# Kernel optimization log

Hardware: AMD Instinct MI355X
Metric: run time of the kernel (lower is better)

The kernel has to match this reference:

```python
import jax, jax.numpy as jnp
import numpy as np

NUM_HEADS = 16
HEAD_DIM = 64
DIM = NUM_HEADS * HEAD_DIM
ROPE_BASE = 10000.0
EPS = 1e-6


def rotate_half(x):
    # pairs (x0,x1) -> (-x1, x0), interleaved on last dim
    x_even = x[..., ::2]
    x_odd = x[..., 1::2]
    return jnp.stack((-x_odd, x_even), axis=-1).reshape(x.shape)


def apply_rope(q, k, positions, base=ROPE_BASE):
    d = q.shape[-1]
    inv_freq = 1.0 / (base ** (jnp.arange(0, d, 2, dtype=jnp.float32) / d))
    angles = positions.astype(jnp.float32)[..., None] * inv_freq  # [B, L, d/2]
    cos = jnp.repeat(jnp.cos(angles), 2, axis=-1).astype(q.dtype)[:, None, :, :]  # [B,1,L,d]
    sin = jnp.repeat(jnp.sin(angles), 2, axis=-1).astype(q.dtype)[:, None, :, :]
    return q * cos + rotate_half(q) * sin, k * cos + rotate_half(k) * sin


def per_head_layernorm(x, weight):
    # x: [B, H, L, d]; weight: [H, d]; bias is zeros (qkv_bias=False)
    mu = jnp.mean(x, axis=-1, keepdims=True)
    var = jnp.mean(jnp.square(x - mu), axis=-1, keepdims=True)
    xn = (x - mu) * jax.lax.rsqrt(var + EPS)
    return xn * weight[None, :, None, :]


def setup_inputs() -> dict:
    key = jax.random.key(0)
    k1, k2, k3, k4, k5 = jax.random.split(key, 5)
    B, L = 2, 2048
    x = jax.random.normal(k1, (B, L, DIM), dtype=jnp.float32)
    mask = jnp.ones((B, L, L), dtype=bool)
    positions = jnp.broadcast_to(jnp.arange(L, dtype=jnp.int64 if jax.config.jax_enable_x64 else jnp.int32), (B, L))
    s = 1.0 / np.sqrt(DIM)
    W_qkv = jax.random.normal(k2, (DIM, 3 * DIM), dtype=jnp.float32) * s
    W_out = jax.random.normal(k3, (DIM, DIM), dtype=jnp.float32) * s
    qn_w = jnp.ones((NUM_HEADS, HEAD_DIM), dtype=jnp.float32)
    kn_w = jnp.ones((NUM_HEADS, HEAD_DIM), dtype=jnp.float32)
    return {"x": x, "mask": mask, "positions": positions,
            "W_qkv": W_qkv, "W_out": W_out, "qn_w": qn_w, "kn_w": kn_w}


def reference(x, mask, positions, W_qkv, W_out, qn_w, kn_w):
    B, L, D = x.shape
    scale = HEAD_DIM ** -0.5
    qkv = x @ W_qkv  # [B, L, 3D]
    qkv = qkv.reshape(B, L, 3, NUM_HEADS, HEAD_DIM)
    qkv = jnp.transpose(qkv, (2, 0, 3, 1, 4))  # [3, B, H, L, d]
    q, k, v = qkv[0], qkv[1], qkv[2]
    q = per_head_layernorm(q, qn_w)
    k = per_head_layernorm(k, kn_w)
    q, k = apply_rope(q, k, positions)
    attn = jnp.einsum('bhqd,bhkd->bhqk', q, k) * scale  # [B, H, L, L]
    attn = jnp.where(mask[:, None, :, :], attn, -jnp.inf)
    attn = jax.nn.softmax(attn, axis=-1)
    out = jnp.einsum('bhqk,bhkd->bhqd', attn, v)  # [B, H, L, d]
    out = jnp.transpose(out, (0, 2, 1, 3)).reshape(B, L, D)
    return out @ W_out
```

## Files before the change

### kernel.cpp

```cpp
#include <hip/hip_runtime.h>


typedef __bf16 bf16x8 __attribute__((ext_vector_type(8)));
typedef __bf16 bf16x2 __attribute__((ext_vector_type(2)));
typedef float f32x4 __attribute__((ext_vector_type(4)));

#define QSCALE 0.1803368802f

__device__ __forceinline__ float bf2f(unsigned short u) {
  unsigned int v = ((unsigned int)u) << 16;
  float f;
  __builtin_memcpy(&f, &v, 4);
  return f;
}
__device__ __forceinline__ unsigned short f2bf(float f) {
  unsigned int v;
  __builtin_memcpy(&v, &f, 4);
  v += 0x7fffu + ((v >> 16) & 1u);
  return (unsigned short)(v >> 16);
}
__device__ __forceinline__ unsigned short f2bf_hw(float f) {
  __bf16 h = (__bf16)f;
  unsigned short u;
  __builtin_memcpy(&u, &h, 2);
  return u;
}
__device__ __forceinline__ unsigned int pack2(float a, float b) {
  bf16x2 t;
  t[0] = (__bf16)a;
  t[1] = (__bf16)b;
  unsigned int u;
  __builtin_memcpy(&u, &t, 4);
  return u;
}
__device__ __forceinline__ void gl_lds16(const unsigned short* g, unsigned short* l) {
  __builtin_amdgcn_global_load_lds(
      (const __attribute__((address_space(1))) unsigned int*)g,
      (__attribute__((address_space(3))) unsigned int*)l, 16, 0, 0);
}

__global__ __launch_bounds__(256) void prep(
    const float* __restrict__ x, const float* __restrict__ W_qkv,
    const float* __restrict__ W_out, const int* __restrict__ positions,
    unsigned short* __restrict__ xb,
    unsigned short* __restrict__ Wt_qkv, unsigned short* __restrict__ Wt_out,
    float2* __restrict__ lut) {
  __shared__ float tile[64][65];
  const int bid = blockIdx.x, t = threadIdx.x;
  if (bid < 4096) {
    int i = (bid * 256 + t) * 4;
    float4 v = *reinterpret_cast<const float4*>(x + i);
    ushort4 o;
    o.x = f2bf(v.x); o.y = f2bf(v.y); o.z = f2bf(v.z); o.w = f2bf(v.w);
    *reinterpret_cast<ushort4*>(xb + i) = o;
    return;
  }
  if (bid >= 5120) {
    int idx = (bid - 5120) * 256 + t;
    int m = idx >> 5, p = idx & 31;
    float pos = (float)positions[m];
    float invf = __builtin_amdgcn_exp2f(-(float)(2 * p) * (13.2877124f / 64.0f));
    float rev = pos * invf * 0.15915494f;
    rev -= floorf(rev);
    lut[idx] = make_float2(__builtin_amdgcn_cosf(rev), __builtin_amdgcn_sinf(rev));
    return;
  }
  const float* W; unsigned short* Wt; int Nd, bn, bk;
  if (bid < 4864) {
    int id = bid - 4096; W = W_qkv; Wt = Wt_qkv; Nd = 3072; bn = id % 48; bk = id / 48;
  } else {
    int id = bid - 4864; W = W_out; Wt = Wt_out; Nd = 1024; bn = id % 16; bk = id / 16;
  }
  const int Kd = 1024;
#pragma unroll
  for (int i = 0; i < 16; i++) {
    int idx = i * 256 + t;
    int k = idx >> 6, n = idx & 63;
    tile[k][n] = W[(size_t)(bk * 64 + k) * Nd + bn * 64 + n];
  }
  __syncthreads();
#pragma unroll
  for (int i = 0; i < 16; i++) {
    int idx = i * 256 + t;
    int n = idx >> 6, k = idx & 63;
    Wt[(size_t)(bn * 64 + n) * Kd + bk * 64 + k] = f2bf(tile[k][n]);
  }
}

__global__ __launch_bounds__(256) void gemm_qkv(
    const unsigned short* __restrict__ A,
    const unsigned short* __restrict__ Bt,
    const float* __restrict__ qn_w, const float* __restrict__ kn_w,
    const float2* __restrict__ lut,
    unsigned short* __restrict__ Qr,
    unsigned short* __restrict__ Kr,
    unsigned short* __restrict__ Vt, int K) {
  __shared__ __align__(16) unsigned short As[128 * 32];
  __shared__ __align__(16) unsigned short Bs[128 * 32];
  const int tid = threadIdx.x;
  const int lane = tid & 63, wid = tid >> 6;
  const int quad = lane >> 4, l16 = lane & 15;
  const int wr = wid >> 1, wc = wid & 1;
  const int bn = blockIdx.x, bm = blockIdx.y;
  const unsigned short* Ab = A + (size_t)bm * 128 * K;
  const unsigned short* Bb = Bt + (size_t)bn * 128 * K;

  f32x4 acc[4][4] = {};

  const int c0 = tid, c1 = tid + 256;
  const int ar0 = c0 >> 2, ag0 = ((c0 & 3) ^ ((ar0 >> 1) & 3)) * 8;
  const int ar1 = c1 >> 2, ag1 = ((c1 & 3) ^ ((ar1 >> 1) & 3)) * 8;

  for (int k0 = 0; k0 < K; k0 += 32) {
    gl_lds16(Ab + (size_t)ar0 * K + k0 + ag0, &As[c0 * 8]);
    gl_lds16(Ab + (size_t)ar1 * K + k0 + ag1, &As[c1 * 8]);
    gl_lds16(Bb + (size_t)ar0 * K + k0 + ag0, &Bs[c0 * 8]);
    gl_lds16(Bb + (size_t)ar1 * K + k0 + ag1, &Bs[c1 * 8]);
    __syncthreads();
    bf16x8 af[4], bfr[4];
#pragma unroll
    for (int i = 0; i < 4; i++) {
      int m = wr * 64 + i * 16 + l16;
      af[i] = *reinterpret_cast<const bf16x8*>(&As[m * 32 + ((quad ^ ((m >> 1) & 3)) * 8)]);
    }
#pragma unroll
    for (int j = 0; j < 4; j++) {
      int n = wc * 64 + j * 16 + l16;
      bfr[j] = *reinterpret_cast<const bf16x8*>(&Bs[n * 32 + ((quad ^ ((n >> 1) & 3)) * 8)]);
    }
#pragma unroll
    for (int i = 0; i < 4; i++)
#pragma unroll
      for (int j = 0; j < 4; j++)
        acc[i][j] = __builtin_amdgcn_mfma_f32_16x16x32_bf16(af[i], bfr[j], acc[i][j], 0, 0, 0);
    __syncthreads();
  }

  const int sec = bn >> 3;
  const int h = (bn & 7) * 2 + wc;
  const int b = bm >> 4;
  if (sec < 2) {
    const float* gw = sec ? kn_w : qn_w;
    unsigned short* dst = sec ? Kr : Qr;
    const float oscale = sec ? 1.0f : QSCALE;
    float w4[4];
#pragma unroll
    for (int j = 0; j < 4; j++) w4[j] = gw[h * 64 + j * 16 + l16];
#pragma unroll
    for (int i = 0; i < 4; i++)
#pragma unroll
      for (int r = 0; r < 4; r++) {
        int m = bm * 128 + wr * 64 + i * 16 + quad * 4 + r;
        int l = m & 2047;
        const float2* lrow = lut + m * 32;
        float2 cs4[4];
#pragma unroll
        for (int j = 0; j < 4; j++) cs4[j] = lrow[j * 8 + (l16 >> 1)];
        float sum = acc[i][0][r] + acc[i][1][r] + acc[i][2][r] + acc[i][3][r];
        float sq = acc[i][0][r] * acc[i][0][r] + acc[i][1][r] * acc[i][1][r] +
                   acc[i][2][r] * acc[i][2][r] + acc[i][3][r] * acc[i][3][r];
#pragma unroll
        for (int off = 1; off < 16; off <<= 1) {
          sum += __shfl_xor(sum, off);
          sq += __shfl_xor(sq, off);
        }
        float mu = sum * (1.0f / 64.0f);
        float var = sq * (1.0f / 64.0f) - mu * mu;
        float rs = rsqrtf(fmaxf(var, 0.0f) + 1e-6f);
#pragma unroll
        for (int j = 0; j < 4; j++) {
          float y = (acc[i][j][r] - mu) * rs * w4[j];
          float p = __shfl_xor(y, 1);
          float o = (l16 & 1) ? (y * cs4[j].x + p * cs4[j].y)
                              : (y * cs4[j].x - p * cs4[j].y);
          dst[((size_t)(b * 16 + h) * 2048 + l) * 64 + j * 16 + l16] = f2bf(o * oscale);
        }
      }
  } else {
#pragma unroll
    for (int i = 0; i < 4; i++) {
      int lp = (bm * 128 + wr * 64 + (i >> 1) * 32 + quad * 8 + (i & 1) * 4) & 2047;
#pragma unroll
      for (int j = 0; j < 4; j++) {
        int d = j * 16 + l16;
        uint2 v;
        v.x = pack2(acc[i][j][0], acc[i][j][1]);
        v.y = pack2(acc[i][j][2], acc[i][j][3]);
        *reinterpret_cast<uint2*>(&Vt[((size_t)(b * 16 + h) * 64 + d) * 2048 + lp]) = v;
      }
    }
  }
}

__global__ __launch_bounds__(512, 4) void attn_kernel(
    const unsigned short* __restrict__ Q,
    const unsigned short* __restrict__ K,
    const unsigned short* __restrict__ Vt,
    unsigned short* __restrict__ O) {
  __shared__ __align__(16) unsigned short Ks[2][2][64 * 64];
  __shared__ __align__(16) unsigned short Vs[2][2][64 * 64];

  int id = blockIdx.x;
  const int qt = id & 15; id >>= 4;
  const int h = id & 15;  const int b = id >> 4;
  const int tid = threadIdx.x;
  const int lane = tid & 63, wid = tid >> 6;
  const int half = wid >> 2, wg = wid & 3;
  const int quad = lane >> 4, l16 = lane & 15;

  const unsigned short* Qb = Q + (size_t)(b * 16 + h) * 2048 * 64;
  const unsigned short* Kb = K + (size_t)(b * 16 + h) * 2048 * 64;
  const unsigned short* Vb = Vt + (size_t)(b * 16 + h) * 64 * 2048;

  const int qbase = qt * 128 + wg * 32;
  bf16x8 qf[2][2];
#pragma unroll
  for (int g = 0; g < 2; g++)
#pragma unroll
    for (int d = 0; d < 2; d++)
      qf[g][d] = *reinterpret_cast<const bf16x8*>(
          &Qb[(size_t)(qbase + g * 16 + l16) * 64 + d * 32 + quad * 8]);

  f32x4 o[2][4] = {};
  float lsum[2] = {0.f, 0.f};

  const int ltid = tid & 255;
  const int c0 = ltid, c1 = ltid + 256;
  const int r0 = c0 >> 3, g0 = ((c0 & 7) ^ (r0 & 7)) * 8;
  const int r1 = c1 >> 3, g1 = ((c1 & 7) ^ (r1 & 7)) * 8;
  const int kb0 = half * 1024;

  gl_lds16(&Kb[(size_t)(kb0 + r0) * 64 + g0], &Ks[half][0][c0 * 8]);
  gl_lds16(&Kb[(size_t)(kb0 + r1) * 64 + g1], &Ks[half][0][c1 * 8]);
  gl_lds16(&Vb[(size_t)r0 * 2048 + kb0 + g0], &Vs[half][0][c0 * 8]);
  gl_lds16(&Vb[(size_t)r1 * 2048 + kb0 + g1], &Vs[half][0][c1 * 8]);

  for (int kt = 0; kt < 16; kt++) {
    const int cur = kt & 1;
    __syncthreads();
    if (kt + 1 < 16) {
      const int ko = kb0 + (kt + 1) * 64, nb = cur ^ 1;
      gl_lds16(&Kb[(size_t)(ko + r0) * 64 + g0], &Ks[half][nb][c0 * 8]);
      gl_lds16(&Kb[(size_t)(ko + r1) * 64 + g1], &Ks[half][nb][c1 * 8]);
      gl_lds16(&Vb[(size_t)r0 * 2048 + ko + g0], &Vs[half][nb][c0 * 8]);
      gl_lds16(&Vb[(size_t)r1 * 2048 + ko + g1], &Vs[half][nb][c1 * 8]);
    }
    const unsigned short* Kc = Ks[half][cur];
    const unsigned short* Vc = Vs[half][cur];

    bf16x8 kf[4][2];
#pragma unroll
    for (int kg = 0; kg < 4; kg++)
#pragma unroll
      for (int d = 0; d < 2; d++) {
        int row = kg * 16 + l16;
        kf[kg][d] = *reinterpret_cast<const bf16x8*>(
            &Kc[row * 64 + (((d * 4 + quad) ^ (row & 7)) * 8)]);
      }
    bf16x8 vf[4][2];
#pragma unroll
    for (int i = 0; i < 4; i++)
#pragma unroll
      for (int c = 0; c < 2; c++) {
        int row = i * 16 + l16;
        vf[i][c] = *reinterpret_cast<const bf16x8*>(
            &Vc[row * 64 + (((c * 4 + quad) ^ (row & 7)) * 8)]);
      }

#pragma unroll
    for (int g = 0; g < 2; g++) {
      f32x4 s4[4] = {};
#pragma unroll
      for (int kg = 0; kg < 4; kg++) {
        s4[kg] = __builtin_amdgcn_mfma_f32_16x16x32_bf16(kf[kg][0], qf[g][0], s4[kg], 0, 0, 0);
        s4[kg] = __builtin_amdgcn_mfma_f32_16x16x32_bf16(kf[kg][1], qf[g][1], s4[kg], 0, 0, 0);
      }
      float pv[4][4];
#pragma unroll
      for (int kg = 0; kg < 4; kg++)
#pragma unroll
        for (int r = 0; r < 4; r++) {
          float e = __builtin_amdgcn_exp2f(s4[kg][r]);
          pv[kg][r] = e;
          lsum[g] += e;
        }
#pragma unroll
      for (int c = 0; c < 2; c++) {
        union { unsigned int u[4]; bf16x8 v; } pa;
        pa.u[0] = pack2(pv[c * 2][0], pv[c * 2][1]);
        pa.u[1] = pack2(pv[c * 2][2], pv[c * 2][3]);
        pa.u[2] = pack2(pv[c * 2 + 1][0], pv[c * 2 + 1][1]);
        pa.u[3] = pack2(pv[c * 2 + 1][2], pv[c * 2 + 1][3]);
#pragma unroll
        for (int i = 0; i < 4; i++)
          o[g][i] = __builtin_amdgcn_mfma_f32_16x16x32_bf16(pa.v, vf[i][c], o[g][i], 0, 0, 0);
      }
    }
  }

#pragma unroll
  for (int g = 0; g < 2; g++) {
    lsum[g] += __shfl_xor(lsum[g], 16);
    lsum[g] += __shfl_xor(lsum[g], 32);
  }

  __syncthreads();
  float* Om = (float*)&Ks[0][0][0];
  float* Lm = (float*)&Vs[0][0][0];
  if (half == 0) {
#pragma unroll
    for (int g = 0; g < 2; g++) {
#pragma unroll
      for (int i = 0; i < 4; i++)
#pragma unroll
        for (int r = 0; r < 4; r++)
          Om[(wg * 32 + g * 16 + quad * 4 + r) * 64 + i * 16 + l16] = o[g][i][r];
      if (quad == 0) Lm[wg * 32 + g * 16 + l16] = lsum[g];
    }
  }
  __syncthreads();
  if (half == 1) {
#pragma unroll
    for (int g = 0; g < 2; g++) {
      float lt = lsum[g] + Lm[wg * 32 + g * 16 + l16];
#pragma unroll
      for (int r = 0; r < 4; r++) {
        float inv = 1.0f / __shfl(lt, quad * 4 + r);
        int q = qbase + g * 16 + quad * 4 + r;
#pragma unroll
        for (int i = 0; i < 4; i++) {
          float sum = o[g][i][r] + Om[(wg * 32 + g * 16 + quad * 4 + r) * 64 + i * 16 + l16];
          O[((size_t)(b * 2048 + q)) * 1024 + h * 64 + i * 16 + l16] = f2bf_hw(sum * inv);
        }
      }
    }
  }
}

__global__ __launch_bounds__(256) void gemm_out(
    const unsigned short* __restrict__ A,
    const unsigned short* __restrict__ Bt,
    float* __restrict__ C, int M, int N, int K) {
  __shared__ __align__(16) unsigned short As[2][128 * 32];
  __shared__ __align__(16) unsigned short Bs[2][64 * 32];
  const int tid = threadIdx.x;
  const int lane = tid & 63, wid = tid >> 6;
  const int quad = lane >> 4, l16 = lane & 15;
  const int bn = blockIdx.x, bm = blockIdx.y;
  const unsigned short* Ab = A + (size_t)bm * 128 * K;
  const unsigned short* Bb = Bt + (size_t)bn * 64 * K;

  f32x4 acc[2][4] = {};

  const int c0 = tid, c1 = tid + 256;
  const int ar0 = c0 >> 2, ag0 = ((c0 & 3) ^ ((ar0 >> 1) & 3)) * 8;
  const int ar1 = c1 >> 2, ag1 = ((c1 & 3) ^ ((ar1 >> 1) & 3)) * 8;
  const int br = tid >> 2, bg = ((tid & 3) ^ ((br >> 1) & 3)) * 8;

  gl_lds16(Ab + (size_t)ar0 * K + ag0, &As[0][c0 * 8]);
  gl_lds16(Ab + (size_t)ar1 * K + ag1, &As[0][c1 * 8]);
  gl_lds16(Bb + (size_t)br * K + bg, &Bs[0][tid * 8]);

  const int iters = K >> 5;
  for (int it = 0; it < iters; it++) {
    const int cur = it & 1;
    __syncthreads();
    if (it + 1 < iters) {
      const int k0 = (it + 1) << 5, nb = cur ^ 1;
      gl_lds16(Ab + (size_t)ar0 * K + k0 + ag0, &As[nb][c0 * 8]);
      gl_lds16(Ab + (size_t)ar1 * K + k0 + ag1, &As[nb][c1 * 8]);
      gl_lds16(Bb + (size_t)br * K + k0 + bg, &Bs[nb][tid * 8]);
    }
    const unsigned short* Ac = As[cur];
    const unsigned short* Bc = Bs[cur];
    bf16x8 af[2], bfr[4];
#pragma unroll
    for (int i = 0; i < 2; i++) {
      int m = wid * 32 + i * 16 + l16;
      af[i] = *reinterpret_cast<const bf16x8*>(&Ac[m * 32 + ((quad ^ ((m >> 1) & 3)) * 8)]);
    }
#pragma unroll
    for (int j = 0; j < 4; j++) {
      int n = j * 16 + l16;
      bfr[j] = *reinterpret_cast<const bf16x8*>(&Bc[n * 32 + ((quad ^ ((n >> 1) & 3)) * 8)]);
    }
#pragma unroll
    for (int i = 0; i < 2; i++)
#pragma unroll
      for (int j = 0; j < 4; j++)
        acc[i][j] = __builtin_amdgcn_mfma_f32_16x16x32_bf16(af[i], bfr[j], acc[i][j], 0, 0, 0);
  }
#pragma unroll
  for (int i = 0; i < 2; i++)
#pragma unroll
    for (int j = 0; j < 4; j++)
#pragma unroll
      for (int r = 0; r < 4; r++) {
        int m = bm * 128 + wid * 32 + i * 16 + quad * 4 + r;
        int n = bn * 64 + j * 16 + l16;
        C[(size_t)m * N + n] = acc[i][j][r];
      }
}

extern "C" void kernel_launch(void* const* d_in, const int* in_sizes, int n_in,
                              void* d_out, int out_size, void* d_ws, size_t ws_size,
                              hipStream_t stream) {
  (void)in_sizes; (void)n_in; (void)out_size; (void)ws_size;
  const float* x     = (const float*)d_in[0];
  const int*   pos   = (const int*)d_in[2];
  const float* W_qkv = (const float*)d_in[3];
  const float* W_out = (const float*)d_in[4];
  const float* qn_w  = (const float*)d_in[5];
  const float* kn_w  = (const float*)d_in[6];
  float*       out   = (float*)d_out;

  char* ws = (char*)d_ws;
  unsigned short* xb     = (unsigned short*)(ws);
  unsigned short* Qr     = (unsigned short*)(ws + 8388608);
  unsigned short* Kr     = (unsigned short*)(ws + 16777216);
  unsigned short* Vt     = (unsigned short*)(ws + 25165824);
  unsigned short* Wt_qkv = (unsigned short*)(ws + 33554432);
  unsigned short* Wt_out = (unsigned short*)(ws + 39845888);
  float2*         lut    = (float2*)(ws + 41943040);
  unsigned short* attn_o = xb;

  prep<<<5632, 256, 0, stream>>>(x, W_qkv, W_out, pos, xb, Wt_qkv, Wt_out, lut);
  gemm_qkv<<<dim3(24, 32), 256, 0, stream>>>(xb, Wt_qkv, qn_w, kn_w, lut, Qr, Kr, Vt, 1024);
  attn_kernel<<<512, 512, 0, stream>>>(Qr, Kr, Vt, attn_o);
  gemm_out<<<dim3(16, 32), 256, 0, stream>>>(attn_o, Wt_out, out, 4096, 1024, 1024);
}
```

Measured before the change: 212.2 us.

## Double-buffer QKV GEMM LDS tiles and compute softmax row sums via MFMA

The QKV projection GEMM now uses double-buffered LDS tiles: the next K-slice is prefetched while MFMAs consume the current one, which also removes one barrier per iteration. In the attention kernel, the per-lane scalar accumulation of exp values plus the final cross-lane shuffles is replaced by an extra MFMA against a vector of ones. That MFMA yields row sums directly in the accumulator layout. The changes double the GEMM's LDS footprint, which may lower occupancy, and the row sums are now built from bf16-rounded probabilities rather than fp32 values.

```diff
diff --git a/kernel.cpp b/kernel.cpp
--- a/kernel.cpp
+++ b/kernel.cpp
@@ -95,8 +95,8 @@
     unsigned short* __restrict__ Qr,
     unsigned short* __restrict__ Kr,
     unsigned short* __restrict__ Vt, int K) {
-  __shared__ __align__(16) unsigned short As[128 * 32];
-  __shared__ __align__(16) unsigned short Bs[128 * 32];
+  __shared__ __align__(16) unsigned short As[2][128 * 32];
+  __shared__ __align__(16) unsigned short Bs[2][128 * 32];
   const int tid = threadIdx.x;
   const int lane = tid & 63, wid = tid >> 6;
   const int quad = lane >> 4, l16 = lane & 15;
@@ -111,29 +111,40 @@
   const int ar0 = c0 >> 2, ag0 = ((c0 & 3) ^ ((ar0 >> 1) & 3)) * 8;
   const int ar1 = c1 >> 2, ag1 = ((c1 & 3) ^ ((ar1 >> 1) & 3)) * 8;
 
-  for (int k0 = 0; k0 < K; k0 += 32) {
-    gl_lds16(Ab + (size_t)ar0 * K + k0 + ag0, &As[c0 * 8]);
-    gl_lds16(Ab + (size_t)ar1 * K + k0 + ag1, &As[c1 * 8]);
-    gl_lds16(Bb + (size_t)ar0 * K + k0 + ag0, &Bs[c0 * 8]);
-    gl_lds16(Bb + (size_t)ar1 * K + k0 + ag1, &Bs[c1 * 8]);
+  gl_lds16(Ab + (size_t)ar0 * K + ag0, &As[0][c0 * 8]);
+  gl_lds16(Ab + (size_t)ar1 * K + ag1, &As[0][c1 * 8]);
+  gl_lds16(Bb + (size_t)ar0 * K + ag0, &Bs[0][c0 * 8]);
+  gl_lds16(Bb + (size_t)ar1 * K + ag1, &Bs[0][c1 * 8]);
+
+  const int iters = K >> 5;
+  for (int it = 0; it < iters; it++) {
+    const int cur = it & 1;
     __syncthreads();
+    if (it + 1 < iters) {
+      const int k0 = (it + 1) << 5, nb = cur ^ 1;
+      gl_lds16(Ab + (size_t)ar0 * K + k0 + ag0, &As[nb][c0 * 8]);
+      gl_lds16(Ab + (size_t)ar1 * K + k0 + ag1, &As[nb][c1 * 8]);
+      gl_lds16(Bb + (size_t)ar0 * K + k0 + ag0, &Bs[nb][c0 * 8]);
+      gl_lds16(Bb + (size_t)ar1 * K + k0 + ag1, &Bs[nb][c1 * 8]);
+    }
+    const unsigned short* Ac = As[cur];
+    const unsigned short* Bc = Bs[cur];
     bf16x8 af[4], bfr[4];
 #pragma unroll
     for (int i = 0; i < 4; i++) {
       int m = wr * 64 + i * 16 + l16;
-      af[i] = *reinterpret_cast<const bf16x8*>(&As[m * 32 + ((quad ^ ((m >> 1) & 3)) * 8)]);
+      af[i] = *reinterpret_cast<const bf16x8*>(&Ac[m * 32 + ((quad ^ ((m >> 1) & 3)) * 8)]);
     }
 #pragma unroll
     for (int j = 0; j < 4; j++) {
       int n = wc * 64 + j * 16 + l16;
-      bfr[j] = *reinterpret_cast<const bf16x8*>(&Bs[n * 32 + ((quad ^ ((n >> 1) & 3)) * 8)]);
+      bfr[j] = *reinterpret_cast<const bf16x8*>(&Bc[n * 32 + ((quad ^ ((n >> 1) & 3)) * 8)]);
     }
 #pragma unroll
     for (int i = 0; i < 4; i++)
 #pragma unroll
       for (int j = 0; j < 4; j++)
         acc[i][j] = __builtin_amdgcn_mfma_f32_16x16x32_bf16(af[i], bfr[j], acc[i][j], 0, 0, 0);
-    __syncthreads();
   }
 
   const int sec = bn >> 3;
@@ -221,8 +232,12 @@
       qf[g][d] = *reinterpret_cast<const bf16x8*>(
           &Qb[(size_t)(qbase + g * 16 + l16) * 64 + d * 32 + quad * 8]);
 
+  bf16x8 ones8;
+#pragma unroll
+  for (int i = 0; i < 8; i++) ones8[i] = (__bf16)1.0f;
+
   f32x4 o[2][4] = {};
-  float lsum[2] = {0.f, 0.f};
+  f32x4 lacc[2] = {};
 
   const int ltid = tid & 255;
   const int c0 = ltid, c1 = ltid + 256;
@@ -279,11 +294,8 @@
 #pragma unroll
       for (int kg = 0; kg < 4; kg++)
 #pragma unroll
-        for (int r = 0; r < 4; r++) {
-          float e = __builtin_amdgcn_exp2f(s4[kg][r]);
-          pv[kg][r] = e;
-          lsum[g] += e;
-        }
+        for (int r = 0; r < 4; r++)
+          pv[kg][r] = __builtin_amdgcn_exp2f(s4[kg][r]);
 #pragma unroll
       for (int c = 0; c < 2; c++) {
         union { unsigned int u[4]; bf16x8 v; } pa;
@@ -291,17 +303,12 @@
         pa.u[1] = pack2(pv[c * 2][2], pv[c * 2][3]);
         pa.u[2] = pack2(pv[c * 2 + 1][0], pv[c * 2 + 1][1]);
         pa.u[3] = pack2(pv[c * 2 + 1][2], pv[c * 2 + 1][3]);
+        lacc[g] = __builtin_amdgcn_mfma_f32_16x16x32_bf16(pa.v, ones8, lacc[g], 0, 0, 0);
 #pragma unroll
         for (int i = 0; i < 4; i++)
           o[g][i] = __builtin_amdgcn_mfma_f32_16x16x32_bf16(pa.v, vf[i][c], o[g][i], 0, 0, 0);
       }
     }
-  }
-
-#pragma unroll
-  for (int g = 0; g < 2; g++) {
-    lsum[g] += __shfl_xor(lsum[g], 16);
-    lsum[g] += __shfl_xor(lsum[g], 32);
   }
 
   __syncthreads();
@@ -315,17 +322,21 @@
 #pragma unroll
         for (int r = 0; r < 4; r++)
           Om[(wg * 32 + g * 16 + quad * 4 + r) * 64 + i * 16 + l16] = o[g][i][r];
-      if (quad == 0) Lm[wg * 32 + g * 16 + l16] = lsum[g];
+      if (l16 == 0) {
+#pragma unroll
+        for (int r = 0; r < 4; r++)
+          Lm[wg * 32 + g * 16 + quad * 4 + r] = lacc[g][r];
+      }
     }
   }
   __syncthreads();
   if (half == 1) {
 #pragma unroll
     for (int g = 0; g < 2; g++) {
-      float lt = lsum[g] + Lm[wg * 32 + g * 16 + l16];
 #pragma unroll
       for (int r = 0; r < 4; r++) {
-        float inv = 1.0f / __shfl(lt, quad * 4 + r);
+        float lt = lacc[g][r] + Lm[wg * 32 + g * 16 + quad * 4 + r];
+        float inv = 1.0f / lt;
         int q = qbase + g * 16 + quad * 4 + r;
 #pragma unroll
         for (int i = 0; i < 4; i++) {
```

Result: no change. 210.5 us (-0.8%).
